# Kernel tuning notes

Hardware: AMD Instinct MI355X
Metric: run time of the kernel (lower is better)

The kernel has to match this reference:

```python
import jax, jax.numpy as jnp
import numpy as np

N_NODES = 25000
N_EDGES = 400000
N_GRAPHS = 64
F_IN = 128


def setup_inputs() -> dict:
    key = jax.random.key(0)
    ks = jax.random.split(key, 16)
    inp = {}
    inp["x"] = jax.random.normal(ks[0], (N_NODES, F_IN), dtype=jnp.float32)
    inp["edge_index"] = jax.random.randint(ks[1], (2, N_EDGES), 0, N_NODES, dtype=jnp.int64)
    inp["edge_attr"] = jax.random.uniform(ks[2], (N_EDGES,), dtype=jnp.float32)
    inp["batch_ids"] = jnp.sort(jax.random.randint(ks[3], (N_NODES,), 0, N_GRAPHS, dtype=jnp.int64))
    def lin(k, fan_in, fan_out):
        bound = 1.0 / np.sqrt(fan_in)
        return jax.random.uniform(k, (fan_in, fan_out), dtype=jnp.float32, minval=-bound, maxval=bound)
    inp["W1_rel"] = lin(ks[4], F_IN, 512)
    inp["b1"] = jnp.zeros((512,), jnp.float32)
    inp["W1_root"] = lin(ks[5], F_IN, 512)
    inp["W2_rel"] = lin(ks[6], 512, 512)
    inp["b2"] = jnp.zeros((512,), jnp.float32)
    inp["W2_root"] = lin(ks[7], 512, 512)
    inp["Wl1"] = lin(ks[8], 512, 64)
    inp["bl1"] = jnp.zeros((64,), jnp.float32)
    inp["Wl2"] = lin(ks[9], 64, 16)
    inp["bl2"] = jnp.zeros((16,), jnp.float32)
    inp["Wl3"] = lin(ks[10], 16, 1)
    inp["bl3"] = jnp.zeros((1,), jnp.float32)
    return inp


def _graph_conv(h, src, dst, edge_attr, W_rel, b_rel, W_root, n_nodes):
    # PyG GraphConv: lin_rel(scatter_add(w_e * x_src, dst)) + lin_root(x)
    msg = h[src] * edge_attr[:, None]                       # [E, F] gather
    agg = jax.ops.segment_sum(msg, dst, num_segments=n_nodes)  # [N, F] scatter-add
    return agg @ W_rel + b_rel + h @ W_root


def reference(x, edge_index, edge_attr, batch_ids, W1_rel, b1, W1_root,
              W2_rel, b2, W2_root, Wl1, bl1, Wl2, bl2, Wl3, bl3):
    n_nodes = x.shape[0]
    src, dst = edge_index[0], edge_index[1]
    h = jax.nn.relu(_graph_conv(x, src, dst, edge_attr, W1_rel, b1, W1_root, n_nodes))
    h = jax.nn.relu(_graph_conv(h, src, dst, edge_attr, W2_rel, b2, W2_root, n_nodes))
    # global mean pool by graph id
    sums = jax.ops.segment_sum(h, batch_ids, num_segments=N_GRAPHS)  # [G, 512]
    counts = jax.ops.segment_sum(jnp.ones((n_nodes,), h.dtype), batch_ids, num_segments=N_GRAPHS)
    g = sums / jnp.maximum(counts, 1.0)[:, None]
    # dropout is identity in eval mode
    g = jax.nn.relu(g @ Wl1 + bl1)
    g = jax.nn.relu(g @ Wl2 + bl2)
    return g @ Wl3 + bl3  # [G, 1]
```

## Files before the change

### kernel.cpp

```cpp
#include <hip/hip_runtime.h>
#include <hip/hip_bf16.h>
#include <hip/hip_fp16.h>
#include <stdint.h>

#define N_NODESC 25000
#define N_EDGESC 400000
#define N_GRAPHSC 64
#define F_INC 128
#define HIDC 512
#define PSTRIDE 1600000
#define MTILES 196

typedef __attribute__((ext_vector_type(8))) short short8;
typedef __attribute__((ext_vector_type(8))) _Float16 half8;
typedef __attribute__((ext_vector_type(4))) float f32x4;

__device__ __forceinline__ unsigned short f2h(float f) {
  return __half_as_ushort(__float2half_rn(f));
}

__global__ __launch_bounds__(256)
void prep_kernel(const float* __restrict__ x, const int* __restrict__ ei,
                 const float* __restrict__ W1rel, const float* __restrict__ W1root,
                 const float* __restrict__ W2rel, const float* __restrict__ W2root,
                 unsigned short* __restrict__ xp, unsigned short* __restrict__ W1T,
                 unsigned short* __restrict__ W2T, int* __restrict__ deg,
                 float* __restrict__ gsum) {
  int blk = blockIdx.x, t = threadIdx.x;
  if (blk < 1563) {
    int e = blk * 256 + t;
    if (e < N_EDGESC) atomicAdd(&deg[ei[N_EDGESC + e]], 1);
  } else if (blk < 4688) {
    int idx = ((blk - 1563) * 256 + t) * 4;
    int node = idx >> 7;
    int col = idx & 127;
    float4 v = *(const float4*)(x + idx);
    ushort4 o;
    o.x = f2h(v.x); o.y = f2h(v.y); o.z = f2h(v.z); o.w = f2h(v.w);
    *(ushort4*)(xp + (size_t)(col >> 6) * PSTRIDE + (size_t)node * 64 + (col & 63)) = o;
  } else if (blk < 4848) {
    __shared__ float tile[64][65];
    int b2 = blk - 4688;
    const float* src;
    unsigned short* dst;
    int n0, k0, Kout;
    if (b2 < 128) {
      int kt = b2 >> 3, nt = b2 & 7;
      k0 = kt * 64; n0 = nt * 64;
      src = (k0 < 512) ? (W2rel + (size_t)k0 * 512) : (W2root + (size_t)(k0 - 512) * 512);
      dst = W2T; Kout = 1024;
    } else {
      int b = b2 - 128;
      int kt = b >> 3, nt = b & 7;
      k0 = kt * 64; n0 = nt * 64;
      src = (k0 < 128) ? (W1rel + (size_t)k0 * 512) : (W1root + (size_t)(k0 - 128) * 512);
      dst = W1T; Kout = 256;
    }
    int c = t & 63;
    int r4 = t >> 6;
#pragma unroll
    for (int rr = 0; rr < 64; rr += 4) {
      int row = rr + r4;
      tile[c][row] = src[(size_t)row * 512 + n0 + c];
    }
    __syncthreads();
#pragma unroll
    for (int rr = 0; rr < 64; rr += 4) {
      int nrow = rr + r4;
      dst[(size_t)(n0 + nrow) * Kout + k0 + c] = f2h(tile[nrow][c]);
    }
  } else {
    int i = (blk - 4848) * 256 + t;
    if (i < N_GRAPHSC * HIDC) gsum[i] = 0.f;
  }
}

__global__ __launch_bounds__(1024)
void scan_kernel(const int* __restrict__ deg, int* __restrict__ indptr, int* __restrict__ cursor,
                 int* __restrict__ sorted) {
  __shared__ int sums[1024];
  __shared__ int bins[256];
  __shared__ int binptr[256];
  const int t = threadIdx.x;
  const int CH = (N_NODESC + 1023) / 1024;
  const int base = t * CH;
  const unsigned ub = (unsigned)deg[N_NODESC];
  if (t < 256) bins[t] = 0;
  __syncthreads();
  int dl[CH];
  int s = 0;
  for (int i = 0; i < CH; ++i) {
    int idx = base + i;
    int d = (idx < N_NODESC) ? (int)((unsigned)deg[idx] - ub) : -1;
    dl[i] = d;
    if (d >= 0) {
      s += d;
      atomicAdd(&bins[d > 255 ? 255 : d], 1);
    }
  }
  sums[t] = s;
  __syncthreads();
  for (int off = 1; off < 1024; off <<= 1) {
    int v = (t >= off) ? sums[t - off] : 0;
    __syncthreads();
    sums[t] += v;
    __syncthreads();
  }
  if (t == 0) {
    int run = 0;
    for (int b = 0; b < 256; ++b) { binptr[b] = run; run += bins[b]; }
  }
  __syncthreads();
  int run = (t > 0) ? sums[t - 1] : 0;
  for (int i = 0; i < CH; ++i) {
    int idx = base + i;
    if (idx < N_NODESC) {
      indptr[idx] = run;
      cursor[idx] = run;
      run += dl[i];
      int pos = atomicAdd(&binptr[dl[i] > 255 ? 255 : dl[i]], 1);
      sorted[pos] = idx;
    }
  }
  if (t == 0) indptr[N_NODESC] = sums[1023];
}

__global__ void fill_kernel(const int* __restrict__ ei, const float* __restrict__ ea,
                            int* __restrict__ cursor, unsigned* __restrict__ emeta) {
  int e = blockIdx.x * blockDim.x + threadIdx.x;
  if (e >= N_EDGESC) return;
  int dst = ei[N_EDGESC + e];
  int pos = atomicAdd(&cursor[dst], 1);
  unsigned short hw = __half_as_ushort(__float2half_rn(ea[e]));
  emeta[pos] = (unsigned)ei[e] | ((unsigned)hw << 16);
}

__global__ __launch_bounds__(256)
void agg_gather_s(const unsigned short* __restrict__ feat, const int* __restrict__ indptr,
                  const unsigned* __restrict__ emeta, const int* __restrict__ sorted,
                  unsigned short* __restrict__ outp, int lgP) {
  int panel = blockIdx.x & ((1 << lgP) - 1);
  int nidx = (blockIdx.x >> lgP) * 32 + (threadIdx.x >> 3);
  if (nidx >= N_NODESC) return;
  int c8 = threadIdx.x & 7;
  int node = sorted[nidx];
  int beg = indptr[node];
  int deg = indptr[node + 1] - beg;
  const unsigned* mp = emeta + beg;
  const char* fb = (const char*)(feat + (size_t)panel * PSTRIDE);
  unsigned coff = c8 * 16u;
  float acc[8] = {};
  int j = 0;
  for (; j + 2 <= deg; j += 2) {
    unsigned mA = mp[j];
    unsigned mB = mp[j + 1];
    half8 vA = *(const half8*)(fb + (mA & 0xffffu) * 128u + coff);
    half8 vB = *(const half8*)(fb + (mB & 0xffffu) * 128u + coff);
    float wA = __half2float(__ushort_as_half((unsigned short)(mA >> 16)));
    float wB = __half2float(__ushort_as_half((unsigned short)(mB >> 16)));
#pragma unroll
    for (int c = 0; c < 8; ++c) acc[c] += (float)vA[c] * wA;
#pragma unroll
    for (int c = 0; c < 8; ++c) acc[c] += (float)vB[c] * wB;
  }
  if (j < deg) {
    unsigned mA = mp[j];
    half8 vA = *(const half8*)(fb + (mA & 0xffffu) * 128u + coff);
    float wA = __half2float(__ushort_as_half((unsigned short)(mA >> 16)));
#pragma unroll
    for (int c = 0; c < 8; ++c) acc[c] += (float)vA[c] * wA;
  }
  half8 o;
#pragma unroll
  for (int c = 0; c < 8; ++c) o[c] = (_Float16)acc[c];
  *(half8*)(outp + (size_t)panel * PSTRIDE + (size_t)node * 64 + c8 * 8) = o;
}

__device__ __forceinline__ void gemm_map(int b, int& m0, int& n0) {
  if (b < 768) {
    int u = b & 7;
    int v = b >> 3;
    m0 = ((v >> 2) * 8 + u) * 128;
    n0 = (v & 3) * 128;
  } else {
    int r = b - 768;
    m0 = (192 + (r >> 2)) * 128;
    n0 = (r & 3) * 128;
  }
}

__global__ __launch_bounds__(256, 3)
void gemm_bt_relu(const short* __restrict__ A0, const short* __restrict__ A1,
                  const short* __restrict__ BT, const float* __restrict__ bias,
                  unsigned short* __restrict__ Outp, int M, int S) {
  const int K = 2 * S;
  __shared__ __align__(16) short As[128 * 64];
  __shared__ __align__(16) short Bs[128 * 64];
  int m0, n0;
  gemm_map(blockIdx.x, m0, n0);
  const int tid = threadIdx.x;
  const int wave = tid >> 6;
  const int lane = tid & 63;
  const int quad = lane >> 4;
  const int r = lane & 15;
  const int wm = (wave >> 1) * 64;
  const int wn = (wave & 1) * 64;

  f32x4 acc[4][4] = {};

  const int nk = K >> 6;
  for (int kt = 0; kt < nk; ++kt) {
    const int kbase = kt << 6;
    const short* Ab;
    int koff;
    if (kbase < S) { Ab = A0; koff = kbase; } else { Ab = A1; koff = kbase - S; }
    const short* Apan = Ab + (size_t)(koff >> 6) * PSTRIDE;
#pragma unroll
    for (int i = 0; i < 4; ++i) {
      int s = ((wave * 4 + i) << 6) + lane;
      int row = s >> 3;
      int c = (s & 7) ^ (row & 7);
      int rg = m0 + row; if (rg > M - 1) rg = M - 1;
      const short* gp = Apan + (size_t)rg * 64 + (c << 3);
      __builtin_amdgcn_global_load_lds((const __attribute__((address_space(1))) void*)gp,
                                       (__attribute__((address_space(3))) void*)&As[(wave * 4 + i) * 512],
                                       16, 0, 0);
    }
#pragma unroll
    for (int i = 0; i < 4; ++i) {
      int s = ((wave * 4 + i) << 6) + lane;
      int row = s >> 3;
      int c = (s & 7) ^ (row & 7);
      const short* gp = BT + (size_t)(n0 + row) * K + kbase + (c << 3);
      __builtin_amdgcn_global_load_lds((const __attribute__((address_space(1))) void*)gp,
                                       (__attribute__((address_space(3))) void*)&Bs[(wave * 4 + i) * 512],
                                       16, 0, 0);
    }
    __syncthreads();
#pragma unroll
    for (int ks = 0; ks < 2; ++ks) {
      half8 af[4], bfr[4];
#pragma unroll
      for (int tm = 0; tm < 4; ++tm) {
        int ml = wm + tm * 16 + r;
        int c = (ks << 2) + quad;
        int slot = ml * 8 + (c ^ (ml & 7));
        af[tm] = *(const half8*)&As[slot * 8];
      }
#pragma unroll
      for (int tn = 0; tn < 4; ++tn) {
        int nl = wn + tn * 16 + r;
        int c = (ks << 2) + quad;
        int slot = nl * 8 + (c ^ (nl & 7));
        bfr[tn] = *(const half8*)&Bs[slot * 8];
      }
#pragma unroll
      for (int tm = 0; tm < 4; ++tm)
#pragma unroll
        for (int tn = 0; tn < 4; ++tn)
          acc[tm][tn] = __builtin_amdgcn_mfma_f32_16x16x32_f16(af[tm], bfr[tn], acc[tm][tn], 0, 0, 0);
    }
    __syncthreads();
  }

#pragma unroll
  for (int tm = 0; tm < 4; ++tm) {
    int rowb = m0 + wm + tm * 16 + quad * 4;
#pragma unroll
    for (int tn = 0; tn < 4; ++tn) {
      int col = n0 + wn + tn * 16 + r;
      float bv = bias[col];
      unsigned short* obase = Outp + (size_t)(col >> 6) * PSTRIDE + (col & 63);
#pragma unroll
      for (int reg = 0; reg < 4; ++reg) {
        int rr = rowb + reg;
        if (rr < M) {
          float v = acc[tm][tn][reg] + bv;
          v = v > 0.f ? v : 0.f;
          obase[(size_t)rr * 64] = f2h(v);
        }
      }
    }
  }
}

__global__ __launch_bounds__(256, 3)
void gemm_bt_pool(const short* __restrict__ A0, const short* __restrict__ A1,
                  const short* __restrict__ BT, const float* __restrict__ bias,
                  const int* __restrict__ batch, float* __restrict__ gsum, int M, int S) {
  const int K = 2 * S;
  __shared__ __align__(16) short As[128 * 64];
  __shared__ __align__(16) short Bs[128 * 64];
  int m0, n0;
  gemm_map(blockIdx.x, m0, n0);
  const int tid = threadIdx.x;
  const int wave = tid >> 6;
  const int lane = tid & 63;
  const int quad = lane >> 4;
  const int r = lane & 15;
  const int wm = (wave >> 1) * 64;
  const int wn = (wave & 1) * 64;

  f32x4 acc[4][4] = {};

  const int nk = K >> 6;
  for (int kt = 0; kt < nk; ++kt) {
    const int kbase = kt << 6;
    const short* Ab;
    int koff;
    if (kbase < S) { Ab = A0; koff = kbase; } else { Ab = A1; koff = kbase - S; }
    const short* Apan = Ab + (size_t)(koff >> 6) * PSTRIDE;
#pragma unroll
    for (int i = 0; i < 4; ++i) {
      int s = ((wave * 4 + i) << 6) + lane;
      int row = s >> 3;
      int c = (s & 7) ^ (row & 7);
      int rg = m0 + row; if (rg > M - 1) rg = M - 1;
      const short* gp = Apan + (size_t)rg * 64 + (c << 3);
      __builtin_amdgcn_global_load_lds((const __attribute__((address_space(1))) void*)gp,
                                       (__attribute__((address_space(3))) void*)&As[(wave * 4 + i) * 512],
                                       16, 0, 0);
    }
#pragma unroll
    for (int i = 0; i < 4; ++i) {
      int s = ((wave * 4 + i) << 6) + lane;
      int row = s >> 3;
      int c = (s & 7) ^ (row & 7);
      const short* gp = BT + (size_t)(n0 + row) * K + kbase + (c << 3);
      __builtin_amdgcn_global_load_lds((const __attribute__((address_space(1))) void*)gp,
                                       (__attribute__((address_space(3))) void*)&Bs[(wave * 4 + i) * 512],
                                       16, 0, 0);
    }
    __syncthreads();
#pragma unroll
    for (int ks = 0; ks < 2; ++ks) {
      half8 af[4], bfr[4];
#pragma unroll
      for (int tm = 0; tm < 4; ++tm) {
        int ml = wm + tm * 16 + r;
        int c = (ks << 2) + quad;
        int slot = ml * 8 + (c ^ (ml & 7));
        af[tm] = *(const half8*)&As[slot * 8];
      }
#pragma unroll
      for (int tn = 0; tn < 4; ++tn) {
        int nl = wn + tn * 16 + r;
        int c = (ks << 2) + quad;
        int slot = nl * 8 + (c ^ (nl & 7));
        bfr[tn] = *(const half8*)&Bs[slot * 8];
      }
#pragma unroll
      for (int tm = 0; tm < 4; ++tm)
#pragma unroll
        for (int tn = 0; tn < 4; ++tn)
          acc[tm][tn] = __builtin_amdgcn_mfma_f32_16x16x32_f16(af[tm], bfr[tn], acc[tm][tn], 0, 0, 0);
    }
    __syncthreads();
  }

  int gid[4][4];
#pragma unroll
  for (int tm = 0; tm < 4; ++tm) {
    int rowb = m0 + wm + tm * 16 + quad * 4;
#pragma unroll
    for (int reg = 0; reg < 4; ++reg) {
      int rr = rowb + reg;
      gid[tm][reg] = batch[rr < M ? rr : (M - 1)];
    }
#pragma unroll
    for (int tn = 0; tn < 4; ++tn) {
      float bv = bias[n0 + wn + tn * 16 + r];
#pragma unroll
      for (int reg = 0; reg < 4; ++reg) {
        int rr = rowb + reg;
        float v = acc[tm][tn][reg] + bv;
        v = v > 0.f ? v : 0.f;
        acc[tm][tn][reg] = (rr < M) ? v : 0.f;
      }
    }
  }
  int g_lo = batch[m0 < M ? m0 : (M - 1)];
  int g_hi = batch[(m0 + 127) < M ? (m0 + 127) : (M - 1)];
  for (int g = g_lo; g <= g_hi; ++g) {
#pragma unroll
    for (int tn = 0; tn < 4; ++tn) {
      float s = 0.f;
#pragma unroll
      for (int tm = 0; tm < 4; ++tm)
#pragma unroll
        for (int reg = 0; reg < 4; ++reg)
          s += (gid[tm][reg] == g) ? acc[tm][tn][reg] : 0.f;
      s += __shfl_xor(s, 16);
      s += __shfl_xor(s, 32);
      if (quad == 0)
        atomicAdd(&gsum[(size_t)g * HIDC + n0 + wn + tn * 16 + r], s);
    }
  }
}

__global__ __launch_bounds__(256)
void mlp_kernel(const float* __restrict__ gsum, const int* __restrict__ batch,
                const float* __restrict__ Wl1, const float* __restrict__ bl1,
                const float* __restrict__ Wl2, const float* __restrict__ bl2,
                const float* __restrict__ Wl3, const float* __restrict__ bl3,
                float* __restrict__ out) {
  int gi = blockIdx.x;
  int t = threadIdx.x;
  int unit = t & 63;
  int part = t >> 6;
  __shared__ float red[4][64];
  __shared__ float h1s[64];
  __shared__ float h2s[16];
  int lo = 0, hi = N_NODESC;
  while (lo < hi) { int mid = (lo + hi) >> 1; if (batch[mid] < gi) lo = mid + 1; else hi = mid; }
  int start = lo;
  hi = N_NODESC;
  while (lo < hi) { int mid = (lo + hi) >> 1; if (batch[mid] < gi + 1) lo = mid + 1; else hi = mid; }
  float inv = 1.0f / fmaxf((float)(lo - start), 1.0f);
  const float* gr = gsum + gi * HIDC;
  float acc = 0.f;
  for (int j = part * 128; j < (part + 1) * 128; ++j)
    acc += gr[j] * Wl1[j * 64 + unit];
  red[part][unit] = acc;
  __syncthreads();
  if (t < 64) {
    float a = bl1[t] + (red[0][t] + red[1][t] + red[2][t] + red[3][t]) * inv;
    h1s[t] = fmaxf(a, 0.f);
  }
  __syncthreads();
  if (t < 16) {
    float a = bl2[t];
    for (int j = 0; j < 64; ++j) a += h1s[j] * Wl2[j * 16 + t];
    h2s[t] = fmaxf(a, 0.f);
  }
  __syncthreads();
  if (t == 0) {
    float a = bl3[0];
    for (int j = 0; j < 16; ++j) a += h2s[j] * Wl3[j];
    out[gi] = a;
  }
}

extern "C" void kernel_launch(void* const* d_in, const int* in_sizes, int n_in,
                              void* d_out, int out_size, void* d_ws, size_t ws_size,
                              hipStream_t stream) {
  const float* x      = (const float*)d_in[0];
  const int*   ei     = (const int*)d_in[1];
  const float* ea     = (const float*)d_in[2];
  const int*   batch  = (const int*)d_in[3];
  const float* W1rel  = (const float*)d_in[4];
  const float* b1     = (const float*)d_in[5];
  const float* W1root = (const float*)d_in[6];
  const float* W2rel  = (const float*)d_in[7];
  const float* b2     = (const float*)d_in[8];
  const float* W2root = (const float*)d_in[9];
  const float* Wl1    = (const float*)d_in[10];
  const float* bl1    = (const float*)d_in[11];
  const float* Wl2    = (const float*)d_in[12];
  const float* bl2    = (const float*)d_in[13];
  const float* Wl3    = (const float*)d_in[14];
  const float* bl3    = (const float*)d_in[15];
  float* out = (float*)d_out;

  char* ws = (char*)d_ws;
  unsigned short* xp     = (unsigned short*)(ws + 0);
  unsigned short* agg1p  = (unsigned short*)(ws + 6400000);
  unsigned short* h1p    = (unsigned short*)(ws + 12800000);
  unsigned short* agg2p  = (unsigned short*)(ws + 38400000);
  unsigned short* W1T    = (unsigned short*)(ws + 64000000);
  unsigned short* W2T    = (unsigned short*)(ws + 64262144);
  float*          gsum   = (float*)(ws + 65310720);
  int*            deg    = (int*)(ws + 65441792);
  int*            cursor = (int*)(ws + 65541796);
  int*            indptr = (int*)(ws + 65641796);
  unsigned*       emeta  = (unsigned*)(ws + 65741812);
  int*            sorted = (int*)(ws + 67341812);

  prep_kernel<<<4976, 256, 0, stream>>>(x, ei, W1rel, W1root, W2rel, W2root,
                                        xp, W1T, W2T, deg, gsum);
  scan_kernel<<<1, 1024, 0, stream>>>(deg, indptr, cursor, sorted);
  fill_kernel<<<(N_EDGESC + 255) / 256, 256, 0, stream>>>(ei, ea, cursor, emeta);

  const int NBLK = (N_NODESC + 31) / 32;
  agg_gather_s<<<NBLK * 2, 256, 0, stream>>>(xp, indptr, emeta, sorted, agg1p, 1);

  gemm_bt_relu<<<784, 256, 0, stream>>>((const short*)agg1p, (const short*)xp,
                                        (const short*)W1T, b1, h1p, N_NODESC, 128);

  agg_gather_s<<<NBLK * 8, 256, 0, stream>>>(h1p, indptr, emeta, sorted, agg2p, 3);

  gemm_bt_pool<<<784, 256, 0, stream>>>((const short*)agg2p, (const short*)h1p,
                                        (const short*)W2T, b2, batch, gsum, N_NODESC, 512);

  mlp_kernel<<<N_GRAPHSC, 256, 0, stream>>>(gsum, batch, Wl1, bl1, Wl2, bl2, Wl3, bl3, out);
}
```

Before: 297.4 us.

## Load GEMM fragments directly from global memory, dropping LDS staging

```diff
diff --git a/kernel.cpp b/kernel.cpp
--- a/kernel.cpp
+++ b/kernel.cpp
@@ -194,8 +194,6 @@
                   const short* __restrict__ BT, const float* __restrict__ bias,
                   unsigned short* __restrict__ Outp, int M, int S) {
   const int K = 2 * S;
-  __shared__ __align__(16) short As[128 * 64];
-  __shared__ __align__(16) short Bs[128 * 64];
   int m0, n0;
   gemm_map(blockIdx.x, m0, n0);
   const int tid = threadIdx.x;
@@ -206,6 +204,17 @@
   const int wm = (wave >> 1) * 64;
   const int wn = (wave & 1) * 64;
 
+  size_t arow[4], brow[4];
+#pragma unroll
+  for (int tm = 0; tm < 4; ++tm) {
+    int rg = m0 + wm + tm * 16 + r;
+    if (rg > M - 1) rg = M - 1;
+    arow[tm] = (size_t)rg * 64 + quad * 8;
+  }
+#pragma unroll
+  for (int tn = 0; tn < 4; ++tn)
+    brow[tn] = (size_t)(n0 + wn + tn * 16 + r) * K + quad * 8;
+
   f32x4 acc[4][4] = {};
 
   const int nk = K >> 6;
@@ -215,52 +224,23 @@
     int koff;
     if (kbase < S) { Ab = A0; koff = kbase; } else { Ab = A1; koff = kbase - S; }
     const short* Apan = Ab + (size_t)(koff >> 6) * PSTRIDE;
-#pragma unroll
-    for (int i = 0; i < 4; ++i) {
-      int s = ((wave * 4 + i) << 6) + lane;
-      int row = s >> 3;
-      int c = (s & 7) ^ (row & 7);
-      int rg = m0 + row; if (rg > M - 1) rg = M - 1;
-      const short* gp = Apan + (size_t)rg * 64 + (c << 3);
-      __builtin_amdgcn_global_load_lds((const __attribute__((address_space(1))) void*)gp,
-                                       (__attribute__((address_space(3))) void*)&As[(wave * 4 + i) * 512],
-                                       16, 0, 0);
-    }
-#pragma unroll
-    for (int i = 0; i < 4; ++i) {
-      int s = ((wave * 4 + i) << 6) + lane;
-      int row = s >> 3;
-      int c = (s & 7) ^ (row & 7);
-      const short* gp = BT + (size_t)(n0 + row) * K + kbase + (c << 3);
-      __builtin_amdgcn_global_load_lds((const __attribute__((address_space(1))) void*)gp,
-                                       (__attribute__((address_space(3))) void*)&Bs[(wave * 4 + i) * 512],
-                                       16, 0, 0);
-    }
-    __syncthreads();
+    half8 af[2][4], bfr[2][4];
 #pragma unroll
     for (int ks = 0; ks < 2; ++ks) {
-      half8 af[4], bfr[4];
-#pragma unroll
-      for (int tm = 0; tm < 4; ++tm) {
-        int ml = wm + tm * 16 + r;
-        int c = (ks << 2) + quad;
-        int slot = ml * 8 + (c ^ (ml & 7));
-        af[tm] = *(const half8*)&As[slot * 8];
-      }
-#pragma unroll
-      for (int tn = 0; tn < 4; ++tn) {
-        int nl = wn + tn * 16 + r;
-        int c = (ks << 2) + quad;
-        int slot = nl * 8 + (c ^ (nl & 7));
-        bfr[tn] = *(const half8*)&Bs[slot * 8];
-      }
 #pragma unroll
       for (int tm = 0; tm < 4; ++tm)
+        af[ks][tm] = *(const half8*)(Apan + arow[tm] + ks * 32);
+#pragma unroll
+      for (int tn = 0; tn < 4; ++tn)
+        bfr[ks][tn] = *(const half8*)(BT + brow[tn] + kbase + ks * 32);
+    }
+#pragma unroll
+    for (int ks = 0; ks < 2; ++ks)
+#pragma unroll
+      for (int tm = 0; tm < 4; ++tm)
 #pragma unroll
         for (int tn = 0; tn < 4; ++tn)
-          acc[tm][tn] = __builtin_amdgcn_mfma_f32_16x16x32_f16(af[tm], bfr[tn], acc[tm][tn], 0, 0, 0);
-    }
-    __syncthreads();
+          acc[tm][tn] = __builtin_amdgcn_mfma_f32_16x16x32_f16(af[ks][tm], bfr[ks][tn], acc[tm][tn], 0, 0, 0);
   }
 
 #pragma unroll
@@ -289,8 +269,6 @@
                   const short* __restrict__ BT, const float* __restrict__ bias,
                   const int* __restrict__ batch, float* __restrict__ gsum, int M, int S) {
   const int K = 2 * S;
-  __shared__ __align__(16) short As[128 * 64];
-  __shared__ __align__(16) short Bs[128 * 64];
   int m0, n0;
   gemm_map(blockIdx.x, m0, n0);
   const int tid = threadIdx.x;
@@ -301,6 +279,17 @@
   const int wm = (wave >> 1) * 64;
   const int wn = (wave & 1) * 64;
 
+  size_t arow[4], brow[4];
+#pragma unroll
+  for (int tm = 0; tm < 4; ++tm) {
+    int rg = m0 + wm + tm * 16 + r;
+    if (rg > M - 1) rg = M - 1;
+    arow[tm] = (size_t)rg * 64 + quad * 8;
+  }
+#pragma unroll
+  for (int tn = 0; tn < 4; ++tn)
+    brow[tn] = (size_t)(n0 + wn + tn * 16 + r) * K + quad * 8;
+
   f32x4 acc[4][4] = {};
 
   const int nk = K >> 6;
@@ -310,52 +299,23 @@
     int koff;
     if (kbase < S) { Ab = A0; koff = kbase; } else { Ab = A1; koff = kbase - S; }
     const short* Apan = Ab + (size_t)(koff >> 6) * PSTRIDE;
-#pragma unroll
-    for (int i = 0; i < 4; ++i) {
-      int s = ((wave * 4 + i) << 6) + lane;
-      int row = s >> 3;
-      int c = (s & 7) ^ (row & 7);
-      int rg = m0 + row; if (rg > M - 1) rg = M - 1;
-      const short* gp = Apan + (size_t)rg * 64 + (c << 3);
-      __builtin_amdgcn_global_load_lds((const __attribute__((address_space(1))) void*)gp,
-                                       (__attribute__((address_space(3))) void*)&As[(wave * 4 + i) * 512],
-                                       16, 0, 0);
-    }
-#pragma unroll
-    for (int i = 0; i < 4; ++i) {
-      int s = ((wave * 4 + i) << 6) + lane;
-      int row = s >> 3;
-      int c = (s & 7) ^ (row & 7);
-      const short* gp = BT + (size_t)(n0 + row) * K + kbase + (c << 3);
-      __builtin_amdgcn_global_load_lds((const __attribute__((address_space(1))) void*)gp,
-                                       (__attribute__((address_space(3))) void*)&Bs[(wave * 4 + i) * 512],
-                                       16, 0, 0);
-    }
-    __syncthreads();
+    half8 af[2][4], bfr[2][4];
 #pragma unroll
     for (int ks = 0; ks < 2; ++ks) {
-      half8 af[4], bfr[4];
-#pragma unroll
-      for (int tm = 0; tm < 4; ++tm) {
-        int ml = wm + tm * 16 + r;
-        int c = (ks << 2) + quad;
-        int slot = ml * 8 + (c ^ (ml & 7));
-        af[tm] = *(const half8*)&As[slot * 8];
-      }
-#pragma unroll
-      for (int tn = 0; tn < 4; ++tn) {
-        int nl = wn + tn * 16 + r;
-        int c = (ks << 2) + quad;
-        int slot = nl * 8 + (c ^ (nl & 7));
-        bfr[tn] = *(const half8*)&Bs[slot * 8];
-      }
 #pragma unroll
       for (int tm = 0; tm < 4; ++tm)
+        af[ks][tm] = *(const half8*)(Apan + arow[tm] + ks * 32);
+#pragma unroll
+      for (int tn = 0; tn < 4; ++tn)
+        bfr[ks][tn] = *(const half8*)(BT + brow[tn] + kbase + ks * 32);
+    }
+#pragma unroll
+    for (int ks = 0; ks < 2; ++ks)
+#pragma unroll
+      for (int tm = 0; tm < 4; ++tm)
 #pragma unroll
         for (int tn = 0; tn < 4; ++tn)
-          acc[tm][tn] = __builtin_amdgcn_mfma_f32_16x16x32_f16(af[tm], bfr[tn], acc[tm][tn], 0, 0, 0);
-    }
-    __syncthreads();
+          acc[tm][tn] = __builtin_amdgcn_mfma_f32_16x16x32_f16(af[ks][tm], bfr[ks][tn], acc[tm][tn], 0, 0, 0);
   }
 
   int gid[4][4];
```

After: 390.7 us. 1.31x slower.
